# Kernel optimization log

Measured on AMD Instinct MI355X. Metric: run time of the kernel, lower is better.

## Reference

```python
import jax, jax.numpy as jnp
import numpy as np

K = 8          # num groups
SIZE = 250     # state/hidden size (h1 = h2 = 250)
M = 576        # flattened input size (24x24)
B = 2048       # batch
HA = 100       # attention hidden
EPS = 1e-5


def _ln(x, g, b):
    mu = jnp.mean(x, axis=-1, keepdims=True)
    v = jnp.mean(jnp.square(x - mu), axis=-1, keepdims=True)
    return (x - mu) * jax.lax.rsqrt(v + EPS) * g + b


def setup_inputs() -> dict:
    key = jax.random.key(0)
    ks = jax.random.split(key, 10)
    def w(k, shape):
        return jax.random.normal(k, shape, jnp.float32) / np.sqrt(shape[0]).astype(np.float32)
    inp = {
        "x": jax.random.normal(ks[0], (B * K, M), jnp.float32),
        "state": jax.random.normal(ks[1], (B * K, SIZE), jnp.float32),
        # encoder: Linear(SIZE,250) + ReLU + LN(250)
        "enc_W": w(ks[2], (SIZE, 250)), "enc_b": jnp.zeros((250,), jnp.float32),
        "enc_g": jnp.ones((250,), jnp.float32), "enc_bt": jnp.zeros((250,), jnp.float32),
        # core: Linear(500,250) + ReLU + LN(250)
        "core_W": w(ks[3], (500, 250)), "core_b": jnp.zeros((250,), jnp.float32),
        "core_g": jnp.ones((250,), jnp.float32), "core_bt": jnp.zeros((250,), jnp.float32),
        # context: Linear(250,250) + ReLU + LN(250)
        "ctx_W": w(ks[4], (250, 250)), "ctx_b": jnp.zeros((250,), jnp.float32),
        "ctx_g": jnp.ones((250,), jnp.float32), "ctx_bt": jnp.zeros((250,), jnp.float32),
        # attention: Linear(250,100)+Tanh+LN(100)+Linear(100,1)+Sigmoid
        "att_W1": w(ks[5], (250, HA)), "att_b1": jnp.zeros((HA,), jnp.float32),
        "att_g": jnp.ones((HA,), jnp.float32), "att_bt": jnp.zeros((HA,), jnp.float32),
        "att_W2": w(ks[6], (HA, 1)), "att_b2": jnp.zeros((1,), jnp.float32),
        # output: Linear(250 + 250 + M, SIZE)
        "out_W": w(ks[7], (250 + 250 + M, SIZE)), "out_b": jnp.zeros((SIZE,), jnp.float32),
    }
    return inp


def reference(x, state, enc_W, enc_b, enc_g, enc_bt, core_W, core_b, core_g, core_bt,
              ctx_W, ctx_b, ctx_g, ctx_bt, att_W1, att_b1, att_g, att_bt,
              att_W2, att_b2, out_W, out_b):
    bk = state.shape[0]
    b = bk // K
    h1 = 250
    # 0-1. encode state -> [B*K, h1]
    s1 = _ln(jax.nn.relu(state @ enc_W + enc_b), enc_g, enc_bt)
    s1r = s1.reshape(b, K, h1)
    # 2-3. focus / context pairs via static gather index [K, K-1]
    idx = np.array([[j for j in range(K) if j != i] for i in range(K)], np.int32)
    cs = s1r[:, idx]                                    # [b, K, K-1, h1]
    fs = jnp.broadcast_to(s1r[:, :, None, :], cs.shape)  # [b, K, K-1, h1]
    # 4. concat pairs -> [b*K*(K-1), 2*h1]
    concat = jnp.concatenate([fs, cs], axis=-1).reshape(b * K * (K - 1), 2 * h1)
    # 5. core MLP
    core_out = _ln(jax.nn.relu(concat @ core_W + core_b), core_g, core_bt)
    # context MLP
    context_out = _ln(jax.nn.relu(core_out @ ctx_W + ctx_b), ctx_g, ctx_bt)
    # attention scalar per pair
    att_h = _ln(jnp.tanh(core_out @ att_W1 + att_b1), att_g, att_bt)
    att = jax.nn.sigmoid(att_h @ att_W2 + att_b2)        # [b*K*(K-1), 1]
    # 6-7. attention-weighted sum over K-1 context effects -> [B*K, h2]
    effect_sum = jnp.sum(context_out.reshape(bk, K - 1, h1) * att.reshape(bk, K - 1, 1), axis=1)
    # 8. decode
    total = jnp.concatenate([s1, effect_sum, x], axis=1)  # [B*K, h1+h2+M]
    new_state = total @ out_W + out_b                     # [B*K, SIZE]
    return new_state
```

## Files before the change

### kernel.cpp

```cpp
#include <hip/hip_runtime.h>
#include <math.h>

#define KK 8
#define H 250
#define MDIM 576
#define NB 2048
#define HA 100
#define ROWS (NB*KK)
#define PROWS (ROWS*7)
#define PQS 512
#define KP 1088
#define EPS 1e-5f

typedef unsigned short ushort_t;
typedef short short8 __attribute__((ext_vector_type(8)));
typedef unsigned short us8 __attribute__((ext_vector_type(8)));
typedef unsigned short us4 __attribute__((ext_vector_type(4)));
typedef unsigned short us2 __attribute__((ext_vector_type(2)));
typedef float f32x4 __attribute__((ext_vector_type(4)));

template<int CTRL>
__device__ __forceinline__ float dpp_add_f32(float x) {
    const int s = __builtin_amdgcn_update_dpp(
        0, __builtin_bit_cast(int, x), CTRL, 0xF, 0xF, true);
    return x + __builtin_bit_cast(float, s);
}
__device__ __forceinline__ float wave_sum_dpp(float x) {
    x = dpp_add_f32<0x111>(x);
    x = dpp_add_f32<0x112>(x);
    x = dpp_add_f32<0x114>(x);
    x = dpp_add_f32<0x118>(x);
    x = dpp_add_f32<0x142>(x);
    x = dpp_add_f32<0x143>(x);
    return __builtin_bit_cast(float, __builtin_amdgcn_readlane(
        __builtin_bit_cast(int, x), 63));
}
__device__ __forceinline__ float bfly16_sum(float x) {
    x = dpp_add_f32<0xB1>(x);
    x = dpp_add_f32<0x4E>(x);
    x = dpp_add_f32<0x141>(x);
    x = dpp_add_f32<0x140>(x);
    return x;
}

__device__ __forceinline__ void async_copy16(const void* g, void* l) {
    __builtin_amdgcn_global_load_lds(
        (const __attribute__((address_space(1))) void*)g,
        (__attribute__((address_space(3))) void*)l, 16, 0, 0);
}

__device__ __forceinline__ ushort_t f2bf(float v) {
    union { float f; unsigned int u; } c; c.f = v;
    unsigned int x = c.u;
    x += 0x7fff + ((x >> 16) & 1);
    return (ushort_t)(x >> 16);
}
__device__ __forceinline__ float bf2f(ushort_t v) {
    union { unsigned int u; float f; } c; c.u = ((unsigned int)v) << 16;
    return c.f;
}
__device__ __forceinline__ float ftanh(float x) {
    const float e = __expf(2.f * x);
    return 1.f - 2.f * __builtin_amdgcn_rcpf(e + 1.f);
}
__device__ __forceinline__ float fsigmoid(float x) {
    return __builtin_amdgcn_rcpf(1.f + __expf(-x));
}

__global__ __launch_bounds__(256) void k_prep(
    const float* __restrict__ out_W, const float* __restrict__ core_W,
    const float* __restrict__ ctx_W, const float* __restrict__ att_W1,
    const float* __restrict__ enc_W, const float* __restrict__ state,
    const float* __restrict__ x,
    ushort_t* __restrict__ Wt, ushort_t* __restrict__ Wpq,
    ushort_t* __restrict__ Wca, ushort_t* __restrict__ Wenc,
    ushort_t* __restrict__ Sb, ushort_t* __restrict__ Abuf)
{
    const int b = blockIdx.x, t = threadIdx.x;
    if (b < 256) {
        const int n = b;
        for (int k = t; k < KP; k += 256) {
            const float v = (n < H && k < 1076) ? out_W[(size_t)k * H + n] : 0.f;
            Wt[(size_t)n * KP + k] = f2bf(v);
        }
    } else if (b < 768) {
        const int n = b - 256, k = t;
        float v = 0.f;
        if (k < H) {
            if (n < H)                    v = core_W[(size_t)k * H + n];
            else if (n >= 256 && n < 506) v = core_W[(size_t)(H + k) * H + (n - 256)];
        }
        Wpq[(size_t)n * 256 + k] = f2bf(v);
    } else if (b < 1152) {
        const int n = b - 768, k = t;
        float v = 0.f;
        if (k < H) {
            if (n < H)           v = ctx_W[(size_t)k * H + n];
            else if (n < H + HA) v = att_W1[(size_t)k * HA + (n - H)];
        }
        Wca[(size_t)n * 256 + k] = f2bf(v);
    } else if (b < 1408) {
        const int n = b - 1152, k = t;
        const float v = (n < H && k < H) ? enc_W[(size_t)k * H + n] : 0.f;
        Wenc[(size_t)n * 256 + k] = f2bf(v);
    } else if (b < 2432) {
        const int r0 = (b - 1408) * 16;
        for (int idx = t; idx < 16 * 256; idx += 256) {
            const int r = r0 + (idx >> 8), k = idx & 255;
            const float v = (k < H) ? state[(size_t)r * H + k] : 0.f;
            Sb[(size_t)r * 256 + k] = f2bf(v);
        }
    } else {
        const int r0 = (b - 2432) * 16;
        for (int idx = t; idx < 16 * 588; idx += 256) {
            const int r = r0 + idx / 588, c = 500 + idx % 588;
            const float v = (c < 500 + MDIM) ? x[(size_t)r * MDIM + (c - 500)] : 0.f;
            Abuf[(size_t)r * KP + c] = f2bf(v);
        }
    }
}

template<int NT>
__global__ __launch_bounds__(512, 4) void k_gemm_nres(
    const ushort_t* __restrict__ A, int lda,
    const ushort_t* __restrict__ B, int ldb,
    void* __restrict__ Cp, int ldc,
    const float* __restrict__ bias,
    int ksteps, int nlim, int bf16out)
{
    constexpr bool DB = (NT <= 4);
    constexpr int NROWS = NT * 64;
    constexpr int ASZ = 32 * 32;
    constexpr int BSZ = NROWS * 32;
    __shared__ __align__(16) ushort_t As[(DB ? 2 : 1) * ASZ];
    __shared__ __align__(16) ushort_t Bs[(DB ? 2 : 1) * BSZ];
    const int tid = threadIdx.x, lane = tid & 63, wave = tid >> 6;
    const int wm = wave >> 2, wn = wave & 3;
    const int R0 = (int)blockIdx.x * 32;

    const int ar = tid >> 2, acb = tid & 3;
    const bool aon = tid < 128;
    const int acl = acb ^ ((ar >> 1) & 3);
    const ushort_t* gA = A + (size_t)(R0 + ar) * lda + acl * 8;

    const int q = lane >> 4, fr = lane & 15;
    const int arow = wm * 16 + fr;

    f32x4 acc[NT] = {};

    if constexpr (DB) {
        auto stage = [&](int ks, int p) {
            const int k0 = ks * 32;
            if (aon) async_copy16(gA + k0, &As[p * ASZ + tid * 8]);
#pragma unroll
            for (int it = 0; it < NT / 2; ++it) {
                const int ci  = it * 512 + tid;
                const int rb  = ci >> 2, cb2 = ci & 3;
                const int clb = cb2 ^ ((rb >> 1) & 3);
                async_copy16(B + (size_t)rb * ldb + k0 + clb * 8,
                             &Bs[p * BSZ + ci * 8]);
            }
        };
        stage(0, 0);
        __syncthreads();
        int p = 0;
        for (int ks = 0; ks < ksteps; ++ks) {
            if (ks + 1 < ksteps) stage(ks + 1, p ^ 1);
            const short8 a = *(const short8*)&As[p * ASZ +
                    (arow * 4 + (q ^ ((arow >> 1) & 3))) * 8];
#pragma unroll
            for (int nt = 0; nt < NT; ++nt) {
                const int n = wn * (NT * 16) + nt * 16 + fr;
                const short8 b = *(const short8*)&Bs[p * BSZ +
                        (n * 4 + (q ^ ((n >> 1) & 3))) * 8];
                acc[nt] = __builtin_amdgcn_mfma_f32_16x16x32_bf16(
                    a, b, acc[nt], 0, 0, 0);
            }
            __syncthreads();
            p ^= 1;
        }
    } else {
        for (int ks = 0; ks < ksteps; ++ks) {
            const int k0 = ks * 32;
            if (aon) async_copy16(gA + k0, &As[tid * 8]);
#pragma unroll
            for (int it = 0; it < NT / 2; ++it) {
                const int ci  = it * 512 + tid;
                const int rb  = ci >> 2, cb2 = ci & 3;
                const int clb = cb2 ^ ((rb >> 1) & 3);
                async_copy16(B + (size_t)rb * ldb + k0 + clb * 8, &Bs[ci * 8]);
            }
            __syncthreads();
            const short8 a = *(const short8*)&As[
                    (arow * 4 + (q ^ ((arow >> 1) & 3))) * 8];
#pragma unroll
            for (int nt = 0; nt < NT; ++nt) {
                const int n = wn * (NT * 16) + nt * 16 + fr;
                const short8 b = *(const short8*)&Bs[(n * 4 + (q ^ ((n >> 1) & 3))) * 8];
                acc[nt] = __builtin_amdgcn_mfma_f32_16x16x32_bf16(
                    a, b, acc[nt], 0, 0, 0);
            }
            __syncthreads();
        }
    }

#pragma unroll
    for (int nt = 0; nt < NT; ++nt) {
        const int col = wn * (NT * 16) + nt * 16 + fr;
        if (col >= nlim) continue;
        const float bv = bias ? bias[col] : 0.f;
#pragma unroll
        for (int reg = 0; reg < 4; ++reg) {
            const int row = R0 + wm * 16 + q * 4 + reg;
            const float v = acc[nt][reg] + bv;
            if (bf16out) ((ushort_t*)Cp)[(size_t)row * ldc + col] = f2bf(v);
            else         ((float*)Cp)[(size_t)row * ldc + col] = v;
        }
    }
}

__global__ __launch_bounds__(256) void k_lnenc(const ushort_t* __restrict__ Epre,
    const float* __restrict__ eb, const float* __restrict__ eg,
    const float* __restrict__ ebt, ushort_t* __restrict__ Abuf)
{
    const int wave = threadIdx.x >> 6, lane = threadIdx.x & 63;
    const int row = blockIdx.x * 4 + wave;
    const int c0 = 4 * lane;

    const us4 v = *(const us4*)&Epre[(size_t)row * 256 + c0];
    float y[4]; float sm = 0.f, sq = 0.f;
#pragma unroll
    for (int t = 0; t < 4; ++t) {
        const int cc = c0 + t;
        float z = 0.f;
        if (cc < H) z = fmaxf(bf2f(v[t]) + eb[cc], 0.f);
        y[t] = z; sm += z; sq += z * z;
    }
    sm = wave_sum_dpp(sm);
    sq = wave_sum_dpp(sq);
    const float mu = sm * (1.f / H);
    const float rs = __builtin_amdgcn_rsqf(sq * (1.f / H) - mu * mu + EPS);
    ushort_t o[4];
#pragma unroll
    for (int t = 0; t < 4; ++t) {
        const int cc = c0 + t;
        o[t] = (cc < H) ? f2bf((y[t] - mu) * rs * eg[cc] + ebt[cc]) : (ushort_t)0;
    }
    ushort_t* dst = Abuf + (size_t)row * KP + c0;
    if (c0 + 3 < H) { *(us4*)dst = (us4){o[0], o[1], o[2], o[3]}; }
    else {
        if (c0 + 1 < H) *(us2*)dst = (us2){o[0], o[1]};
    }
}

__global__ __launch_bounds__(256) void k_core(const ushort_t* __restrict__ PQb,
    const float* __restrict__ core_b, const float* __restrict__ core_g,
    const float* __restrict__ core_bt, ushort_t* __restrict__ Co)
{
    const int wave = threadIdx.x >> 6, lane = threadIdx.x & 63;
    const int g = blockIdx.x * 4 + wave;
    const int i = g & 7;
    const int c = lane * 4;

    const us4 pu = *(const us4*)&PQb[(size_t)g * PQS + c];
    us4 qu[7];
#pragma unroll
    for (int jj = 0; jj < 7; ++jj) {
        const int j = jj + (jj >= i ? 1 : 0);
        const int qr = (g & ~7) + j;
        qu[jj] = *(const us4*)&PQb[(size_t)qr * PQS + 256 + c];
    }
    float pe[4], cb[4], cg[4], cbt[4]; bool vl[4];
#pragma unroll
    for (int t = 0; t < 4; ++t) {
        vl[t]  = (c + t) < H;
        pe[t]  = bf2f(pu[t]);
        cb[t]  = vl[t] ? core_b[c + t]  : 0.f;
        cg[t]  = vl[t] ? core_g[c + t]  : 0.f;
        cbt[t] = vl[t] ? core_bt[c + t] : 0.f;
    }
    float z[7][4], red[7][2];
#pragma unroll
    for (int jj = 0; jj < 7; ++jj) {
        float sm = 0.f, sq = 0.f;
#pragma unroll
        for (int t = 0; t < 4; ++t) {
            const float zz = vl[t] ? fmaxf(pe[t] + bf2f(qu[jj][t]) + cb[t], 0.f) : 0.f;
            z[jj][t] = zz; sm += zz; sq = fmaf(zz, zz, sq);
        }
        red[jj][0] = sm; red[jj][1] = sq;
    }
#pragma unroll
    for (int jj = 0; jj < 7; ++jj) {
        red[jj][0] = wave_sum_dpp(red[jj][0]);
        red[jj][1] = wave_sum_dpp(red[jj][1]);
    }
#pragma unroll
    for (int jj = 0; jj < 7; ++jj) {
        const float mu = red[jj][0] * (1.f / H);
        const float rs = __builtin_amdgcn_rsqf(red[jj][1] * (1.f / H) - mu * mu + EPS);
        us4 o;
#pragma unroll
        for (int t = 0; t < 4; ++t)
            o[t] = vl[t] ? f2bf((z[jj][t] - mu) * rs * cg[t] + cbt[t]) : (ushort_t)0;
        *(us4*)&Co[((size_t)g * 7 + jj) * 256 + c] = o;
    }
}

__global__ __launch_bounds__(512, 4) void k_cs(
    const ushort_t* __restrict__ Co,
    const ushort_t* __restrict__ Wca,
    const float* __restrict__ ctx_b,
    const float* __restrict__ att_b1, const float* __restrict__ att_g,
    const float* __restrict__ attW2,
    ushort_t* __restrict__ Cs, float* __restrict__ Srow)
{
    __shared__ __align__(16) ushort_t As[64 * 32];
    __shared__ __align__(16) ushort_t Bs[384 * 32];
    const int tid = threadIdx.x, lane = tid & 63, wave = tid >> 6;
    const int wmm = wave >> 2, wnn = wave & 3;
    const int R0 = (int)blockIdx.x * 64;

    const int ar = tid >> 2, acb = tid & 3;
    const bool aon = tid < 256;
    const int acl = acb ^ ((ar >> 1) & 3);
    const ushort_t* gA = Co + (size_t)(R0 + ar) * 256 + acl * 8;

    const int q = lane >> 4, fr = lane & 15;

    f32x4 acc[2][6] = {};
    for (int ks = 0; ks < 8; ++ks) {
        const int k0 = ks * 32;
        if (aon) async_copy16(gA + k0, &As[tid * 8]);
#pragma unroll
        for (int it = 0; it < 3; ++it) {
            const int ci  = it * 512 + tid;
            const int rb  = ci >> 2, cb2 = ci & 3;
            const int clb = cb2 ^ ((rb >> 1) & 3);
            async_copy16(Wca + (size_t)rb * 256 + k0 + clb * 8, &Bs[ci * 8]);
        }
        __syncthreads();
        short8 a[2];
#pragma unroll
        for (int ms = 0; ms < 2; ++ms) {
            const int row = wmm * 32 + ms * 16 + fr;
            a[ms] = *(const short8*)&As[(row * 4 + (q ^ ((row >> 1) & 3))) * 8];
        }
#pragma unroll
        for (int nt = 0; nt < 6; ++nt) {
            const int n = wnn * 96 + nt * 16 + fr;
            const short8 b = *(const short8*)&Bs[(n * 4 + (q ^ ((n >> 1) & 3))) * 8];
#pragma unroll
            for (int ms = 0; ms < 2; ++ms)
                acc[ms][nt] = __builtin_amdgcn_mfma_f32_16x16x32_bf16(
                    a[ms], b, acc[ms][nt], 0, 0, 0);
        }
        __syncthreads();
    }

    bool eC[6], eA[6]; float b_[6], gw[6];
#pragma unroll
    for (int nt = 0; nt < 6; ++nt) {
        const int col = wnn * 96 + nt * 16 + fr;
        eC[nt] = col < H;
        eA[nt] = (col >= H) && (col < H + HA);
        if (eC[nt])      { b_[nt] = ctx_b[col];      gw[nt] = 0.f; }
        else if (eA[nt]) { const int ca = col - H;
                           b_[nt] = att_b1[ca];
                           gw[nt] = att_g[ca] * attW2[ca]; }
        else             { b_[nt] = gw[nt] = 0.f; }
    }

#pragma unroll
    for (int ms = 0; ms < 2; ++ms) {
        float smc[4] = {}, sqc[4] = {}, sma[4] = {}, sqa[4] = {}, szgw[4] = {};
#pragma unroll
        for (int nt = 0; nt < 6; ++nt) {
#pragma unroll
            for (int reg = 0; reg < 4; ++reg) {
                const float val = acc[ms][nt][reg] + b_[nt];
                if (eC[nt]) {
                    const float zz = fmaxf(val, 0.f);
                    acc[ms][nt][reg] = zz;
                    smc[reg] += zz; sqc[reg] = fmaf(zz, zz, sqc[reg]);
                } else if (eA[nt]) {
                    const float za = ftanh(val);
                    sma[reg] += za; sqa[reg] = fmaf(za, za, sqa[reg]);
                    szgw[reg] = fmaf(za, gw[nt], szgw[reg]);
                }
            }
        }
#pragma unroll
        for (int reg = 0; reg < 4; ++reg) {
            smc[reg]  = bfly16_sum(smc[reg]);
            sqc[reg]  = bfly16_sum(sqc[reg]);
            sma[reg]  = bfly16_sum(sma[reg]);
            sqa[reg]  = bfly16_sum(sqa[reg]);
            szgw[reg] = bfly16_sum(szgw[reg]);
        }
        if (fr == 0) {
#pragma unroll
            for (int reg = 0; reg < 4; ++reg) {
                const int row = R0 + wmm * 32 + ms * 16 + q * 4 + reg;
                *(f32x4*)&Srow[(size_t)row * 32 + wnn * 8] =
                    (f32x4){smc[reg], sqc[reg], sma[reg], sqa[reg]};
                Srow[(size_t)row * 32 + wnn * 8 + 4] = szgw[reg];
            }
        }
#pragma unroll
        for (int nt = 0; nt < 6; ++nt) {
            const int col = wnn * 96 + nt * 16 + fr;
            if (col >= 256) continue;
#pragma unroll
            for (int reg = 0; reg < 4; ++reg) {
                const int row = R0 + wmm * 32 + ms * 16 + q * 4 + reg;
                Cs[(size_t)row * 256 + col] =
                    eC[nt] ? f2bf(acc[ms][nt][reg]) : (ushort_t)0;
            }
        }
    }
}

__global__ __launch_bounds__(256) void k_eff2(
    const ushort_t* __restrict__ Cs, const float* __restrict__ Srow,
    const float* __restrict__ ctx_g, const float* __restrict__ ctx_bt,
    const float* __restrict__ att_g, const float* __restrict__ att_bt,
    const float* __restrict__ attW2, const float* __restrict__ att_b2,
    ushort_t* __restrict__ Abuf)
{
    const int wave = threadIdx.x >> 6, lane = threadIdx.x & 63;
    const int g = blockIdx.x * 4 + wave;
    const int c0 = 4 * lane;

    float psg = 0.f, psb = 0.f;
    for (int c = lane; c < HA; c += 64) {
        const float w2 = attW2[c];
        psg = fmaf(att_g[c], w2, psg);
        psb = fmaf(att_bt[c], w2, psb);
    }
    psg = wave_sum_dpp(psg); psb = wave_sum_dpp(psb);
    const float sgw = psg;
    const float ab2 = att_b2[0] + psb;

    float g4[4], bt4[4];
#pragma unroll
    for (int t = 0; t < 4; ++t) {
        const bool vl = (c0 + t) < H;
        g4[t]  = vl ? ctx_g[c0 + t]  : 0.f;
        bt4[t] = vl ? ctx_bt[c0 + t] : 0.f;
    }

    us4 zv[7];
#pragma unroll
    for (int jj = 0; jj < 7; ++jj)
        zv[jj] = *(const us4*)&Cs[((size_t)g * 7 + jj) * 256 + c0];

    float A4[4] = {0.f, 0.f, 0.f, 0.f};
    float S0 = 0.f, S1 = 0.f;
#pragma unroll
    for (int jj = 0; jj < 7; ++jj) {
        const float* sr = Srow + ((size_t)g * 7 + jj) * 32;
        float s0 = 0.f, s1 = 0.f, s2 = 0.f, s3 = 0.f, s4 = 0.f;
#pragma unroll
        for (int w = 0; w < 4; ++w) {
            const f32x4 v = *(const f32x4*)&sr[w * 8];
            s0 += v[0]; s1 += v[1]; s2 += v[2]; s3 += v[3];
            s4 += sr[w * 8 + 4];
        }
        const float muC = s0 * (1.f / H);
        const float rsC = __builtin_amdgcn_rsqf(s1 * (1.f / H) - muC * muC + EPS);
        const float muA = s2 * (1.f / HA);
        const float rsA = __builtin_amdgcn_rsqf(s3 * (1.f / HA) - muA * muA + EPS);
        const float dot = rsA * (s4 - muA * sgw) + ab2;
        const float ag  = fsigmoid(dot);
        const float cj  = ag * rsC;
        S0 += ag; S1 = fmaf(cj, muC, S1);
#pragma unroll
        for (int e = 0; e < 4; ++e)
            A4[e] = fmaf(cj, bf2f(zv[jj][e]), A4[e]);
    }
    ushort_t o[4];
#pragma unroll
    for (int e = 0; e < 4; ++e)
        o[e] = f2bf(g4[e] * (A4[e] - S1) + bt4[e] * S0);
    ushort_t* dst = Abuf + (size_t)g * KP + H + c0;
    if (c0 + 1 < H) *(us2*)dst       = (us2){o[0], o[1]};
    if (c0 + 3 < H) *(us2*)(dst + 2) = (us2){o[2], o[3]};
}

extern "C" void kernel_launch(void* const* d_in, const int* in_sizes, int n_in,
                              void* d_out, int out_size, void* d_ws, size_t ws_size,
                              hipStream_t stream)
{
    const float* x      = (const float*)d_in[0];
    const float* state  = (const float*)d_in[1];
    const float* enc_W  = (const float*)d_in[2];
    const float* enc_b  = (const float*)d_in[3];
    const float* enc_g  = (const float*)d_in[4];
    const float* enc_bt = (const float*)d_in[5];
    const float* core_W = (const float*)d_in[6];
    const float* core_b = (const float*)d_in[7];
    const float* core_g = (const float*)d_in[8];
    const float* core_bt= (const float*)d_in[9];
    const float* ctx_W  = (const float*)d_in[10];
    const float* ctx_b  = (const float*)d_in[11];
    const float* ctx_g  = (const float*)d_in[12];
    const float* ctx_bt = (const float*)d_in[13];
    const float* att_W1 = (const float*)d_in[14];
    const float* att_b1 = (const float*)d_in[15];
    const float* att_g  = (const float*)d_in[16];
    const float* att_bt = (const float*)d_in[17];
    const float* att_W2 = (const float*)d_in[18];
    const float* att_b2 = (const float*)d_in[19];
    const float* out_W  = (const float*)d_in[20];
    const float* out_b  = (const float*)d_in[21];
    float* out = (float*)d_out;

    ushort_t* Abuf = (ushort_t*)d_ws;
    ushort_t* Wt   = Abuf + (size_t)ROWS * KP;
    ushort_t* Wpq  = Wt + (size_t)256 * KP;
    ushort_t* Wca  = Wpq + (size_t)512 * 256;
    ushort_t* Wenc = Wca + (size_t)384 * 256;
    ushort_t* Co   = Wenc + (size_t)256 * 256;
    ushort_t* Cs   = Co + (size_t)PROWS * 256;
    float*    Srow = (float*)(Cs + (size_t)PROWS * 256);
    ushort_t* Sb   = Cs;
    ushort_t* Epre = Sb + (size_t)ROWS * 256;
    ushort_t* PQb  = Epre + (size_t)ROWS * 256;

    k_prep  <<<3456, 256, 0, stream>>>(out_W, core_W, ctx_W, att_W1, enc_W,
                                       state, x, Wt, Wpq, Wca, Wenc, Sb, Abuf);
    k_gemm_nres<4><<<ROWS / 32, 512, 0, stream>>>(Sb, 256, Wenc, 256, Epre, 256,
                                                  nullptr, 8, 256, 1);
    k_lnenc <<<ROWS / 4, 256, 0, stream>>>(Epre, enc_b, enc_g, enc_bt, Abuf);
    k_gemm_nres<8><<<ROWS / 32, 512, 0, stream>>>(Abuf, KP, Wpq, 256, PQb, PQS,
                                                  nullptr, 8, 512, 1);
    k_core  <<<ROWS / 4, 256, 0, stream>>>(PQb, core_b, core_g, core_bt, Co);
    k_cs    <<<PROWS / 64, 512, 0, stream>>>(Co, Wca, ctx_b, att_b1, att_g,
                                             att_W2, Cs, Srow);
    k_eff2  <<<ROWS / 4, 256, 0, stream>>>(Cs, Srow, ctx_g, ctx_bt,
                                           att_g, att_bt, att_W2, att_b2, Abuf);
    k_gemm_nres<4><<<ROWS / 32, 512, 0, stream>>>(Abuf, KP, Wt, KP, out, H,
                                                  out_b, KP / 32, 250, 0);
}
```

Before: 334.3 us.

## Fuse encoder GEMM with bias/ReLU/LayerNorm and skip dead reductions in k_cs

Replaces the separate encoder GEMM and LayerNorm kernels with one kernel. It computes the 32-row GEMM tile with MFMA, then applies bias, ReLU and a cross-wave LayerNorm reduction through shared memory before writing bf16 to Abuf. This removes a kernel launch and the Epre intermediate round trip. In k_cs, the butterfly reductions and Cs stores now run only in the waves whose columns hold context or attention outputs, skipping work on zeros. The trade-off is that the fused kernel uses more shared memory and adds block-level synchronisation.

```diff
diff --git a/kernel.cpp b/kernel.cpp
--- a/kernel.cpp
+++ b/kernel.cpp
@@ -219,37 +219,113 @@
     }
 }
 
-__global__ __launch_bounds__(256) void k_lnenc(const ushort_t* __restrict__ Epre,
+__global__ __launch_bounds__(512, 4) void k_encln(
+    const ushort_t* __restrict__ Sb,
+    const ushort_t* __restrict__ Wenc,
     const float* __restrict__ eb, const float* __restrict__ eg,
-    const float* __restrict__ ebt, ushort_t* __restrict__ Abuf)
+    const float* __restrict__ ebt,
+    ushort_t* __restrict__ Abuf)
 {
-    const int wave = threadIdx.x >> 6, lane = threadIdx.x & 63;
-    const int row = blockIdx.x * 4 + wave;
-    const int c0 = 4 * lane;
-
-    const us4 v = *(const us4*)&Epre[(size_t)row * 256 + c0];
-    float y[4]; float sm = 0.f, sq = 0.f;
-#pragma unroll
-    for (int t = 0; t < 4; ++t) {
-        const int cc = c0 + t;
-        float z = 0.f;
-        if (cc < H) z = fmaxf(bf2f(v[t]) + eb[cc], 0.f);
-        y[t] = z; sm += z; sq += z * z;
-    }
-    sm = wave_sum_dpp(sm);
-    sq = wave_sum_dpp(sq);
-    const float mu = sm * (1.f / H);
-    const float rs = __builtin_amdgcn_rsqf(sq * (1.f / H) - mu * mu + EPS);
-    ushort_t o[4];
-#pragma unroll
-    for (int t = 0; t < 4; ++t) {
-        const int cc = c0 + t;
-        o[t] = (cc < H) ? f2bf((y[t] - mu) * rs * eg[cc] + ebt[cc]) : (ushort_t)0;
-    }
-    ushort_t* dst = Abuf + (size_t)row * KP + c0;
-    if (c0 + 3 < H) { *(us4*)dst = (us4){o[0], o[1], o[2], o[3]}; }
-    else {
-        if (c0 + 1 < H) *(us2*)dst = (us2){o[0], o[1]};
+    constexpr int ASZ = 32 * 32;
+    constexpr int BSZ = 256 * 32;
+    __shared__ __align__(16) ushort_t As[2 * ASZ];
+    __shared__ __align__(16) ushort_t Bs[2 * BSZ];
+    const int tid = threadIdx.x, lane = tid & 63, wave = tid >> 6;
+    const int wm = wave >> 2, wn = wave & 3;
+    const int R0 = (int)blockIdx.x * 32;
+
+    const int ar = tid >> 2, acb = tid & 3;
+    const bool aon = tid < 128;
+    const int acl = acb ^ ((ar >> 1) & 3);
+    const ushort_t* gA = Sb + (size_t)(R0 + ar) * 256 + acl * 8;
+
+    const int q = lane >> 4, fr = lane & 15;
+    const int arow = wm * 16 + fr;
+
+    auto stage = [&](int ks, int p) {
+        const int k0 = ks * 32;
+        if (aon) async_copy16(gA + k0, &As[p * ASZ + tid * 8]);
+#pragma unroll
+        for (int it = 0; it < 2; ++it) {
+            const int ci  = it * 512 + tid;
+            const int rb  = ci >> 2, cb2 = ci & 3;
+            const int clb = cb2 ^ ((rb >> 1) & 3);
+            async_copy16(Wenc + (size_t)rb * 256 + k0 + clb * 8,
+                         &Bs[p * BSZ + ci * 8]);
+        }
+    };
+
+    f32x4 acc[4] = {};
+    stage(0, 0);
+    __syncthreads();
+    int p = 0;
+    for (int ks = 0; ks < 8; ++ks) {
+        if (ks + 1 < 8) stage(ks + 1, p ^ 1);
+        const short8 a = *(const short8*)&As[p * ASZ +
+                (arow * 4 + (q ^ ((arow >> 1) & 3))) * 8];
+#pragma unroll
+        for (int nt = 0; nt < 4; ++nt) {
+            const int n = wn * 64 + nt * 16 + fr;
+            const short8 b = *(const short8*)&Bs[p * BSZ +
+                    (n * 4 + (q ^ ((n >> 1) & 3))) * 8];
+            acc[nt] = __builtin_amdgcn_mfma_f32_16x16x32_bf16(a, b, acc[nt], 0, 0, 0);
+        }
+        __syncthreads();
+        p ^= 1;
+    }
+
+    float* red  = (float*)Bs;
+    float* scal = (float*)Bs + 256;
+
+    float y[4][4]; float sm[4] = {}, sq[4] = {};
+#pragma unroll
+    for (int nt = 0; nt < 4; ++nt) {
+        const int col = wn * 64 + nt * 16 + fr;
+        const float ebv = (col < H) ? eb[col] : 0.f;
+#pragma unroll
+        for (int reg = 0; reg < 4; ++reg) {
+            float z = 0.f;
+            if (col < H) z = fmaxf(acc[nt][reg] + ebv, 0.f);
+            y[nt][reg] = z; sm[reg] += z; sq[reg] = fmaf(z, z, sq[reg]);
+        }
+    }
+#pragma unroll
+    for (int reg = 0; reg < 4; ++reg) {
+        sm[reg] = bfly16_sum(sm[reg]);
+        sq[reg] = bfly16_sum(sq[reg]);
+    }
+    if (fr == 0) {
+#pragma unroll
+        for (int reg = 0; reg < 4; ++reg) {
+            const int row = wm * 16 + q * 4 + reg;
+            red[row * 8 + wn * 2]     = sm[reg];
+            red[row * 8 + wn * 2 + 1] = sq[reg];
+        }
+    }
+    __syncthreads();
+    if (wave == 0 && lane < 32) {
+        const float s0 = red[lane * 8]     + red[lane * 8 + 2] +
+                         red[lane * 8 + 4] + red[lane * 8 + 6];
+        const float s1 = red[lane * 8 + 1] + red[lane * 8 + 3] +
+                         red[lane * 8 + 5] + red[lane * 8 + 7];
+        const float mu = s0 * (1.f / H);
+        const float rs = __builtin_amdgcn_rsqf(s1 * (1.f / H) - mu * mu + EPS);
+        scal[lane * 2]     = mu;
+        scal[lane * 2 + 1] = rs;
+    }
+    __syncthreads();
+#pragma unroll
+    for (int nt = 0; nt < 4; ++nt) {
+        const int col = wn * 64 + nt * 16 + fr;
+        if (col >= H) continue;
+        const float egv = eg[col], ebtv = ebt[col];
+#pragma unroll
+        for (int reg = 0; reg < 4; ++reg) {
+            const int row = wm * 16 + q * 4 + reg;
+            const float mu = scal[row * 2], rs = scal[row * 2 + 1];
+            Abuf[(size_t)(R0 + row) * KP + col] =
+                f2bf((y[nt][reg] - mu) * rs * egv + ebtv);
+        }
     }
 }
 
@@ -390,13 +466,20 @@
                 }
             }
         }
-#pragma unroll
-        for (int reg = 0; reg < 4; ++reg) {
-            smc[reg]  = bfly16_sum(smc[reg]);
-            sqc[reg]  = bfly16_sum(sqc[reg]);
-            sma[reg]  = bfly16_sum(sma[reg]);
-            sqa[reg]  = bfly16_sum(sqa[reg]);
-            szgw[reg] = bfly16_sum(szgw[reg]);
+        if (wnn <= 2) {
+#pragma unroll
+            for (int reg = 0; reg < 4; ++reg) {
+                smc[reg] = bfly16_sum(smc[reg]);
+                sqc[reg] = bfly16_sum(sqc[reg]);
+            }
+        }
+        if (wnn >= 2) {
+#pragma unroll
+            for (int reg = 0; reg < 4; ++reg) {
+                sma[reg]  = bfly16_sum(sma[reg]);
+                sqa[reg]  = bfly16_sum(sqa[reg]);
+                szgw[reg] = bfly16_sum(szgw[reg]);
+            }
         }
         if (fr == 0) {
 #pragma unroll
@@ -407,15 +490,17 @@
                 Srow[(size_t)row * 32 + wnn * 8 + 4] = szgw[reg];
             }
         }
-#pragma unroll
-        for (int nt = 0; nt < 6; ++nt) {
-            const int col = wnn * 96 + nt * 16 + fr;
-            if (col >= 256) continue;
-#pragma unroll
-            for (int reg = 0; reg < 4; ++reg) {
-                const int row = R0 + wmm * 32 + ms * 16 + q * 4 + reg;
-                Cs[(size_t)row * 256 + col] =
-                    eC[nt] ? f2bf(acc[ms][nt][reg]) : (ushort_t)0;
+        if (wnn <= 2) {
+#pragma unroll
+            for (int nt = 0; nt < 6; ++nt) {
+                const int col = wnn * 96 + nt * 16 + fr;
+                if (col >= 256) continue;
+#pragma unroll
+                for (int reg = 0; reg < 4; ++reg) {
+                    const int row = R0 + wmm * 32 + ms * 16 + q * 4 + reg;
+                    Cs[(size_t)row * 256 + col] =
+                        eC[nt] ? f2bf(acc[ms][nt][reg]) : (ushort_t)0;
+                }
             }
         }
     }
@@ -530,9 +615,7 @@
 
     k_prep  <<<3456, 256, 0, stream>>>(out_W, core_W, ctx_W, att_W1, enc_W,
                                        state, x, Wt, Wpq, Wca, Wenc, Sb, Abuf);
-    k_gemm_nres<4><<<ROWS / 32, 512, 0, stream>>>(Sb, 256, Wenc, 256, Epre, 256,
-                                                  nullptr, 8, 256, 1);
-    k_lnenc <<<ROWS / 4, 256, 0, stream>>>(Epre, enc_b, enc_g, enc_bt, Abuf);
+    k_encln <<<ROWS / 32, 512, 0, stream>>>(Sb, Wenc, enc_b, enc_g, enc_bt, Abuf);
     k_gemm_nres<8><<<ROWS / 32, 512, 0, stream>>>(Abuf, KP, Wpq, 256, PQb, PQS,
                                                   nullptr, 8, 512, 1);
     k_core  <<<ROWS / 4, 256, 0, stream>>>(PQb, core_b, core_g, core_bt, Co);
```

Measured after the change: 319.2 us. 1.05x faster.
